# Kernel optimization log

Measured on AMD Instinct MI355X. Metric: run time of the kernel, lower is better.

Reference implementation:

```python
import jax, jax.numpy as jnp
import numpy as np

N, E = 50000, 600000
IN_DIM, HID, OUT_DIM = 128, 256, 64


def _sage_conv(x, edge_index, W_l, W_r, b):
    # PyG SAGEConv (mean aggr, root_weight=True):
    # out = mean_{j in N(i)} x_j @ W_l + x_i @ W_r + b
    src, dst = edge_index[0], edge_index[1]
    msg = x[src]  # [E, d] gather
    agg = jax.ops.segment_sum(msg, dst, num_segments=N)  # [N, d]
    cnt = jax.ops.segment_sum(jnp.ones((E,), dtype=x.dtype), dst, num_segments=N)
    agg = agg / jnp.maximum(cnt, 1.0)[:, None]
    return agg @ W_l + x @ W_r + b


def setup_inputs() -> dict:
    key = jax.random.key(0)
    ks = jax.random.split(key, 8)
    x = jax.random.normal(ks[0], (N, IN_DIM), dtype=jnp.float32)
    edge_index = jax.random.randint(ks[1], (2, E), 0, N, dtype=jnp.int64)
    s1 = 1.0 / np.sqrt(IN_DIM)
    s2 = 1.0 / np.sqrt(HID)
    W1_l = jax.random.uniform(ks[2], (IN_DIM, HID), jnp.float32, -s1, s1)
    W1_r = jax.random.uniform(ks[3], (IN_DIM, HID), jnp.float32, -s1, s1)
    b1 = jnp.zeros((HID,), jnp.float32)
    W2_l = jax.random.uniform(ks[4], (HID, OUT_DIM), jnp.float32, -s2, s2)
    W2_r = jax.random.uniform(ks[5], (HID, OUT_DIM), jnp.float32, -s2, s2)
    b2 = jnp.zeros((OUT_DIM,), jnp.float32)
    return {"x": x, "edge_index": edge_index, "W1_l": W1_l, "W1_r": W1_r,
            "b1": b1, "W2_l": W2_l, "W2_r": W2_r, "b2": b2}


def reference(x, edge_index, W1_l, W1_r, b1, W2_l, W2_r, b2):
    # SAGE.forward, eval mode (dropout = identity)
    h = jax.nn.relu(_sage_conv(x, edge_index, W1_l, W1_r, b1))
    out = _sage_conv(h, edge_index, W2_l, W2_r, b2)
    return out
```

## Files before the change

kernel.cpp:

```cpp
#include <hip/hip_runtime.h>

#define N_NODES 50000
#define N_EDGES 600000
#define N_PAD   50048
#define IN_DIM 128
#define HID 256
#define OUT_DIM 64
#define MAX_DEG 64
#define NBINS 196
#define BCAP 4096
#define NPART 256
#define ECHUNK 2344
#define EPT 10

typedef __attribute__((ext_vector_type(4))) float f32x4;
typedef __attribute__((ext_vector_type(8))) short short8;
typedef unsigned short u16;
typedef unsigned int u32;

__device__ __forceinline__ float bf2f(u32 lo16) {
  u32 u = lo16 << 16;
  return __builtin_bit_cast(float, u);
}
__device__ __forceinline__ u16 f2bf(float f) {
  u32 u = __builtin_bit_cast(u32, f);
  u = (u + 0x7FFF + ((u >> 16) & 1)) >> 16;
  return (u16)u;
}


__global__ void k_zero_gcur(int* __restrict__ gcur) {
  gcur[threadIdx.x] = 0;
}

#define SEG0 (N_PAD * 16)
#define SEG1 (SEG0 + 128 * 64)
#define SEG2 (SEG1 + 64 * 64)
#define PREP_TOT SEG2

__global__ void k_prep_part(const float* __restrict__ x,
                            const float* __restrict__ W1l, const float* __restrict__ W1r,
                            const float* __restrict__ W2l, const float* __restrict__ W2r,
                            const int* __restrict__ src, const int* __restrict__ dst,
                            u16* __restrict__ xb, u16* __restrict__ W1p,
                            u16* __restrict__ W2p, u32* __restrict__ region,
                            int* __restrict__ gcur) {
  if (blockIdx.x < NPART) {
    __shared__ int hist[256];
    __shared__ int base[256];
    const int t = threadIdx.x;
    hist[t] = 0;
    __syncthreads();
    const int e0 = blockIdx.x * ECHUNK;
    const int e1 = min(e0 + ECHUNK, N_EDGES);
    int dv[EPT], sv[EPT];
#pragma unroll
    for (int i = 0; i < EPT; ++i) {
      int e = e0 + t + i * 256;
      int ok = (e < e1);
      dv[i] = ok ? dst[e] : -1;
      sv[i] = ok ? src[e] : 0;
      if (ok) atomicAdd(&hist[dv[i] >> 8], 1);
    }
    __syncthreads();
    base[t] = (hist[t] > 0) ? atomicAdd(&gcur[t], hist[t]) : 0;
    hist[t] = 0;
    __syncthreads();
#pragma unroll
    for (int i = 0; i < EPT; ++i) {
      int d = dv[i];
      if (d >= 0) {
        int bin = d >> 8;
        int idx = base[bin] + atomicAdd(&hist[bin], 1);
        if (idx < BCAP)
          region[(size_t)bin * BCAP + idx] = (u32)(sv[i] & 0xffff) | ((u32)(d & 255) << 16);
      }
    }
    return;
  }
  int idx = (blockIdx.x - NPART) * 256 + threadIdx.x;
  if (idx < SEG0) {
    int row = idx >> 4;
    int c8 = (idx & 15) * 8;
    short8 o;
    if (row < N_NODES) {
      f32x4 a = *(const f32x4*)&x[(size_t)row * 128 + c8];
      f32x4 b = *(const f32x4*)&x[(size_t)row * 128 + c8 + 4];
      o[0] = (short)f2bf(a[0]); o[1] = (short)f2bf(a[1]);
      o[2] = (short)f2bf(a[2]); o[3] = (short)f2bf(a[3]);
      o[4] = (short)f2bf(b[0]); o[5] = (short)f2bf(b[1]);
      o[6] = (short)f2bf(b[2]); o[7] = (short)f2bf(b[3]);
    } else {
      for (int j = 0; j < 8; ++j) o[j] = 0;
    }
    *(short8*)&xb[(size_t)row * 128 + c8] = o;
  } else if (idx < SEG1) {
    int i = idx - SEG0;
    int F = i >> 6, l = i & 63;
    int wch = F >> 6, kt = (F >> 4) & 3, kk = (F >> 3) & 1, n = F & 7;
    int row = wch * 128 + n * 16 + (l & 15);
    int kb = kt * 64 + kk * 32 + (l >> 4) * 8;
    short8 o;
#pragma unroll
    for (int j = 0; j < 8; ++j) {
      int k = kb + j;
      float v = (k < 128) ? W1l[(size_t)k * HID + row] : W1r[(size_t)(k - 128) * HID + row];
      o[j] = (short)f2bf(v);
    }
    *(short8*)&W1p[(size_t)i * 8] = o;
  } else if (idx < SEG2) {
    int i = idx - SEG1;
    int G = i >> 6, l = i & 63;
    int wch = G >> 5, kk = (G >> 2) & 7, n = G & 3;
    int row = wch * 64 + n * 16 + (l & 15);
    int kb = kk * 32 + (l >> 4) * 8;
    short8 o;
#pragma unroll
    for (int j = 0; j < 8; ++j) {
      int k = kb + j;
      float v = (row < 64) ? W2l[(size_t)k * OUT_DIM + row]
                           : W2r[(size_t)k * OUT_DIM + (row - 64)];
      o[j] = (short)f2bf(v);
    }
    *(short8*)&W2p[(size_t)i * 8] = o;
  }
}


__global__ __launch_bounds__(256) void k_build(const u32* __restrict__ region,
                                               const int* __restrict__ gcur,
                                               int* __restrict__ cnt,
                                               u16* __restrict__ bucket) {
  __shared__ u16 lbkt[256 * 64];
  __shared__ int lcnt[256];
  const int t = threadIdx.x;
  const int bin = blockIdx.x;
  lcnt[t] = 0;
  __syncthreads();
  int n = gcur[bin];
  if (n > BCAP) n = BCAP;
  for (int i = t; i < n; i += 256) {
    u32 r = region[(size_t)bin * BCAP + i];
    int dl = (r >> 16) & 255;
    int pos = atomicAdd(&lcnt[dl], 1);
    if (pos < MAX_DEG) lbkt[dl * 64 + pos] = (u16)(r & 0xffff);
  }
  __syncthreads();
  int gnode = bin * 256 + t;
  if (gnode < N_NODES) cnt[gnode] = lcnt[t];
  for (int i = t; i < 2048; i += 256) {
    int nl = i >> 3, sub = i & 7;
    int gn = bin * 256 + nl;
    if (gn < N_NODES)
      *(short8*)&bucket[(size_t)gn * 64 + sub * 8] = *(const short8*)&lbkt[nl * 64 + sub * 8];
  }
}


__global__ void k_agg(const u16* __restrict__ xb, const int* __restrict__ cnt,
                      const u16* __restrict__ bucket, u16* __restrict__ agg) {
  int node = blockIdx.x * 4 + (threadIdx.x >> 6);
  if (node >= N_PAD) return;
  int lane = threadIdx.x & 63;
  int es = lane >> 4, dl = lane & 15;
  int deg = (node < N_NODES) ? cnt[node] : 0;
  int sreg = (node < N_NODES) ? (int)bucket[(size_t)node * MAX_DEG + lane] : 0;
  float acc[8] = {0.f, 0.f, 0.f, 0.f, 0.f, 0.f, 0.f, 0.f};
  short8 pend = (short8){0, 0, 0, 0, 0, 0, 0, 0};
  for (int e = 0; e < deg; e += 4) {
    int ee = e + es;
    int s = __shfl(sreg, ee & 63);
    short8 v = (short8){0, 0, 0, 0, 0, 0, 0, 0};
    if (ee < deg) v = *(const short8*)&xb[(size_t)s * 128 + dl * 8];
#pragma unroll
    for (int j = 0; j < 8; ++j) acc[j] += bf2f((u16)pend[j]);
    pend = v;
  }
#pragma unroll
  for (int j = 0; j < 8; ++j) acc[j] += bf2f((u16)pend[j]);
#pragma unroll
  for (int j = 0; j < 8; ++j) {
    acc[j] += __shfl_xor(acc[j], 16);
    acc[j] += __shfl_xor(acc[j], 32);
  }
  float inv = 1.f / fmaxf((float)deg, 1.f);
  if (es == 0) {
    short8 o;
#pragma unroll
    for (int j = 0; j < 8; ++j) o[j] = (short)f2bf(acc[j] * inv);
    *(short8*)&agg[(size_t)node * 128 + dl * 8] = o;
  }
}


__device__ __forceinline__ void gl_lds16(const void* g, void* l) {
  __builtin_amdgcn_global_load_lds((const __attribute__((address_space(1))) u32*)g,
                                   (__attribute__((address_space(3))) u32*)l, 16, 0, 0);
}

__global__ __launch_bounds__(256, 3) void k_mlp(
    const u16* __restrict__ agg, const u16* __restrict__ xb,
    const u16* __restrict__ W1p, const u16* __restrict__ W2p,
    const float* __restrict__ b1, u16* __restrict__ pb, u16* __restrict__ qb) {
  __shared__ u16 hs[64 * 256];
  __shared__ u16 As[2][64 * 64];
  const int t = threadIdx.x;
  const int wave = t >> 6;
  const int lane = t & 63;
  const int brow = blockIdx.x * 64;
  const int lr = lane & 15;
  const int kg = lane >> 4;
  const int wch = wave & 1;

  const int wr = (wave >> 1) * 32;
  const int wc = wch * 128;

  f32x4 acc[2][8];
#pragma unroll
  for (int m = 0; m < 2; ++m)
#pragma unroll
    for (int n = 0; n < 8; ++n) acc[m][n] = (f32x4){0.f, 0.f, 0.f, 0.f};

  auto stageA = [&](int buf, int kt) {
    const u16* base = (kt < 2) ? agg : xb;
    const int koff = (kt & 1) * 64;
#pragma unroll
    for (int i = 0; i < 2; ++i) {
      int chunk = wave * 2 + i;
      int f = chunk * 1024 + lane * 16;
      int row = f >> 7;
      int cbs = (f & 127) ^ ((row & 7) << 4);
      gl_lds16(&base[(size_t)(brow + row) * 128 + koff + (cbs >> 1)],
               (char*)As[buf] + chunk * 1024);
    }
  };

  stageA(0, 0);
  __syncthreads();

#pragma unroll
  for (int kt = 0; kt < 4; ++kt) {
    const int cur = kt & 1;
    if (kt < 3) stageA(cur ^ 1, kt + 1);
#pragma unroll
    for (int kk = 0; kk < 2; ++kk) {
      short8 af[2], bfr[8];
      const int cb = kk * 64 + kg * 16;
#pragma unroll
      for (int m = 0; m < 2; ++m) {
        int row = wr + m * 16 + lr;
        af[m] = *(const short8*)((const char*)As[cur] + row * 128 + (cb ^ ((row & 7) << 4)));
      }
#pragma unroll
      for (int n = 0; n < 8; ++n)
        bfr[n] = *(const short8*)&W1p[(size_t)(((wch * 4 + kt) * 2 + kk) * 8 + n) * 512 +
                                      lane * 8];
#pragma unroll
      for (int m = 0; m < 2; ++m)
#pragma unroll
        for (int n = 0; n < 8; ++n)
          acc[m][n] =
              __builtin_amdgcn_mfma_f32_16x16x32_bf16(af[m], bfr[n], acc[m][n], 0, 0, 0);
    }
    __syncthreads();
  }

#pragma unroll
  for (int n = 0; n < 8; ++n) {
    int col = wc + n * 16 + lr;
    float bv = b1[col];
#pragma unroll
    for (int m = 0; m < 2; ++m) {
#pragma unroll
      for (int j = 0; j < 4; ++j) {
        int row = wr + kg * 4 + m * 16 + j;
        float v = fmaxf(acc[m][n][j] + bv, 0.f);
        *(u16*)((char*)hs + row * 512 + ((col * 2) ^ ((row & 7) << 4))) = f2bf(v);
      }
    }
  }
  __syncthreads();

  const int wr2 = (wave >> 1) * 32;
  f32x4 acc2[2][4];
#pragma unroll
  for (int m = 0; m < 2; ++m)
#pragma unroll
    for (int n = 0; n < 4; ++n) acc2[m][n] = (f32x4){0.f, 0.f, 0.f, 0.f};

#pragma unroll
  for (int kk = 0; kk < 8; ++kk) {
    const int cb = kk * 64 + kg * 16;
    short8 af[2], bfr[4];
#pragma unroll
    for (int m = 0; m < 2; ++m) {
      int row = wr2 + m * 16 + lr;
      af[m] = *(const short8*)((const char*)hs + row * 512 + (cb ^ ((row & 7) << 4)));
    }
#pragma unroll
    for (int n = 0; n < 4; ++n)
      bfr[n] = *(const short8*)&W2p[(size_t)((wch * 8 + kk) * 4 + n) * 512 + lane * 8];
#pragma unroll
    for (int m = 0; m < 2; ++m)
#pragma unroll
      for (int n = 0; n < 4; ++n)
        acc2[m][n] =
            __builtin_amdgcn_mfma_f32_16x16x32_bf16(af[m], bfr[n], acc2[m][n], 0, 0, 0);
  }

  u16* outb = wch ? qb : pb;
#pragma unroll
  for (int n = 0; n < 4; ++n) {
    int col = n * 16 + lr;
#pragma unroll
    for (int m = 0; m < 2; ++m) {
#pragma unroll
      for (int j = 0; j < 4; ++j) {
        int row = brow + wr2 + kg * 4 + m * 16 + j;
        outb[(size_t)row * 64 + col] = f2bf(acc2[m][n][j]);
      }
    }
  }
}


__global__ void k_out(const u16* __restrict__ pb, const u16* __restrict__ qb,
                      const int* __restrict__ cnt, const u16* __restrict__ bucket,
                      const float* __restrict__ b2, float* __restrict__ out) {
  int node = blockIdx.x * 4 + (threadIdx.x >> 6);
  if (node >= N_NODES) return;
  int lane = threadIdx.x & 63;
  int es = lane >> 3, dl = lane & 7;
  int deg = cnt[node];
  int sreg = (int)bucket[(size_t)node * MAX_DEG + lane];
  float acc[8] = {0.f, 0.f, 0.f, 0.f, 0.f, 0.f, 0.f, 0.f};
  short8 pend = (short8){0, 0, 0, 0, 0, 0, 0, 0};
  for (int e = 0; e < deg; e += 8) {
    int ee = e + es;
    int s = __shfl(sreg, ee & 63);
    short8 v = (short8){0, 0, 0, 0, 0, 0, 0, 0};
    if (ee < deg) v = *(const short8*)&pb[(size_t)s * 64 + dl * 8];
#pragma unroll
    for (int j = 0; j < 8; ++j) acc[j] += bf2f((u16)pend[j]);
    pend = v;
  }
#pragma unroll
  for (int j = 0; j < 8; ++j) acc[j] += bf2f((u16)pend[j]);
#pragma unroll
  for (int j = 0; j < 8; ++j) {
    acc[j] += __shfl_xor(acc[j], 8);
    acc[j] += __shfl_xor(acc[j], 16);
    acc[j] += __shfl_xor(acc[j], 32);
  }
  float inv = 1.f / fmaxf((float)deg, 1.f);
  if (es == 0) {
    short8 q = *(const short8*)&qb[(size_t)node * 64 + dl * 8];
    f32x4 bb0 = *(const f32x4*)&b2[dl * 8];
    f32x4 bb1 = *(const f32x4*)&b2[dl * 8 + 4];
    f32x4 o0, o1;
#pragma unroll
    for (int j = 0; j < 4; ++j) {
      o0[j] = acc[j] * inv + bf2f((u16)q[j]) + bb0[j];
      o1[j] = acc[j + 4] * inv + bf2f((u16)q[j + 4]) + bb1[j];
    }
    *(f32x4*)&out[(size_t)node * 64 + dl * 8] = o0;
    *(f32x4*)&out[(size_t)node * 64 + dl * 8 + 4] = o1;
  }
}


extern "C" void kernel_launch(void* const* d_in, const int* in_sizes, int n_in,
                              void* d_out, int out_size, void* d_ws, size_t ws_size,
                              hipStream_t stream) {
  const float* x   = (const float*)d_in[0];
  const int*   ei  = (const int*)d_in[1];
  const float* W1l = (const float*)d_in[2];
  const float* W1r = (const float*)d_in[3];
  const float* b1  = (const float*)d_in[4];
  const float* W2l = (const float*)d_in[5];
  const float* W2r = (const float*)d_in[6];
  const float* b2  = (const float*)d_in[7];
  float* out = (float*)d_out;

  const int* src = ei;
  const int* dst = ei + N_EDGES;

  char* ws = (char*)d_ws;
  size_t off = 0;
  auto alloc = [&](size_t bytes) -> void* {
    void* p = ws + off;
    off = (off + bytes + 255) & ~(size_t)255;
    return p;
  };
  int* gcur   = (int*)alloc(256 * 4);
  u32* region = (u32*)alloc((size_t)NBINS * BCAP * 4);
  int* cnt    = (int*)alloc((size_t)N_NODES * 4);
  u16* bucket = (u16*)alloc((size_t)N_NODES * MAX_DEG * 2);
  u16* xb     = (u16*)alloc((size_t)N_PAD * 128 * 2);
  u16* agg    = (u16*)alloc((size_t)N_PAD * 128 * 2);
  u16* W1p    = (u16*)alloc((size_t)128 * 64 * 8 * 2);
  u16* W2p    = (u16*)alloc((size_t)64 * 64 * 8 * 2);
  u16* pb     = (u16*)alloc((size_t)N_PAD * 64 * 2);
  u16* qb     = (u16*)alloc((size_t)N_PAD * 64 * 2);

  k_zero_gcur<<<1, 256, 0, stream>>>(gcur);

  int blocks = NPART + (PREP_TOT + 255) / 256;
  k_prep_part<<<blocks, 256, 0, stream>>>(x, W1l, W1r, W2l, W2r, src, dst,
                                          xb, W1p, W2p, region, gcur);
  k_build<<<NBINS, 256, 0, stream>>>(region, gcur, cnt, bucket);
  k_agg<<<N_PAD / 4, 256, 0, stream>>>(xb, cnt, bucket, agg);
  k_mlp<<<N_PAD / 64, 256, 0, stream>>>(agg, xb, W1p, W2p, b1, pb, qb);
  k_out<<<(N_NODES + 3) / 4, 256, 0, stream>>>(pb, qb, cnt, bucket, b2, out);
}
```

Before: 98.84 us.

## Load MLP A operands directly from global and trim bucket reads/writes to degree

The first-layer GEMM in k_mlp no longer stages A tiles through double-buffered LDS with global_load_lds. Each wave now reads its A fragments straight from global memory, which removes the per-k-step barriers and frees LDS so the launch-bounds occupancy hint can rise from 3 to 5. Separately, the bucket scatter writes only the 8-wide chunks that hold valid neighbors, and the aggregation kernels read bucket entries only for lanes below the node degree, cutting memory traffic on the sparse side. The risk is that several waves now fetch the same A rows from global without LDS reuse, and that register pressure at the higher occupancy target could cause spills.

```diff
diff --git a/kernel.cpp b/kernel.cpp
--- a/kernel.cpp
+++ b/kernel.cpp
@@ -151,7 +151,7 @@
   for (int i = t; i < 2048; i += 256) {
     int nl = i >> 3, sub = i & 7;
     int gn = bin * 256 + nl;
-    if (gn < N_NODES)
+    if (gn < N_NODES && sub * 8 < lcnt[nl])
       *(short8*)&bucket[(size_t)gn * 64 + sub * 8] = *(const short8*)&lbkt[nl * 64 + sub * 8];
   }
 }
@@ -164,7 +164,7 @@
   int lane = threadIdx.x & 63;
   int es = lane >> 4, dl = lane & 15;
   int deg = (node < N_NODES) ? cnt[node] : 0;
-  int sreg = (node < N_NODES) ? (int)bucket[(size_t)node * MAX_DEG + lane] : 0;
+  int sreg = (lane < deg) ? (int)bucket[(size_t)node * MAX_DEG + lane] : 0;
   float acc[8] = {0.f, 0.f, 0.f, 0.f, 0.f, 0.f, 0.f, 0.f};
   short8 pend = (short8){0, 0, 0, 0, 0, 0, 0, 0};
   for (int e = 0; e < deg; e += 4) {
@@ -193,17 +193,11 @@
 }
 
 
-__device__ __forceinline__ void gl_lds16(const void* g, void* l) {
-  __builtin_amdgcn_global_load_lds((const __attribute__((address_space(1))) u32*)g,
-                                   (__attribute__((address_space(3))) u32*)l, 16, 0, 0);
-}
-
-__global__ __launch_bounds__(256, 3) void k_mlp(
+__global__ __launch_bounds__(256, 5) void k_mlp(
     const u16* __restrict__ agg, const u16* __restrict__ xb,
     const u16* __restrict__ W1p, const u16* __restrict__ W2p,
     const float* __restrict__ b1, u16* __restrict__ pb, u16* __restrict__ qb) {
   __shared__ u16 hs[64 * 256];
-  __shared__ u16 As[2][64 * 64];
   const int t = threadIdx.x;
   const int wave = t >> 6;
   const int lane = t & 63;
@@ -221,35 +215,17 @@
 #pragma unroll
     for (int n = 0; n < 8; ++n) acc[m][n] = (f32x4){0.f, 0.f, 0.f, 0.f};
 
-  auto stageA = [&](int buf, int kt) {
-    const u16* base = (kt < 2) ? agg : xb;
+#pragma unroll
+  for (int kt = 0; kt < 4; ++kt) {
+    const u16* Abase = (kt < 2) ? agg : xb;
     const int koff = (kt & 1) * 64;
-#pragma unroll
-    for (int i = 0; i < 2; ++i) {
-      int chunk = wave * 2 + i;
-      int f = chunk * 1024 + lane * 16;
-      int row = f >> 7;
-      int cbs = (f & 127) ^ ((row & 7) << 4);
-      gl_lds16(&base[(size_t)(brow + row) * 128 + koff + (cbs >> 1)],
-               (char*)As[buf] + chunk * 1024);
-    }
-  };
-
-  stageA(0, 0);
-  __syncthreads();
-
-#pragma unroll
-  for (int kt = 0; kt < 4; ++kt) {
-    const int cur = kt & 1;
-    if (kt < 3) stageA(cur ^ 1, kt + 1);
 #pragma unroll
     for (int kk = 0; kk < 2; ++kk) {
       short8 af[2], bfr[8];
-      const int cb = kk * 64 + kg * 16;
 #pragma unroll
       for (int m = 0; m < 2; ++m) {
-        int row = wr + m * 16 + lr;
-        af[m] = *(const short8*)((const char*)As[cur] + row * 128 + (cb ^ ((row & 7) << 4)));
+        int row = brow + wr + m * 16 + lr;
+        af[m] = *(const short8*)&Abase[(size_t)row * 128 + koff + kk * 32 + kg * 8];
       }
 #pragma unroll
       for (int n = 0; n < 8; ++n)
@@ -262,7 +238,6 @@
           acc[m][n] =
               __builtin_amdgcn_mfma_f32_16x16x32_bf16(af[m], bfr[n], acc[m][n], 0, 0, 0);
     }
-    __syncthreads();
   }
 
 #pragma unroll
@@ -332,7 +307,7 @@
   int lane = threadIdx.x & 63;
   int es = lane >> 3, dl = lane & 7;
   int deg = cnt[node];
-  int sreg = (int)bucket[(size_t)node * MAX_DEG + lane];
+  int sreg = (lane < deg) ? (int)bucket[(size_t)node * MAX_DEG + lane] : 0;
   float acc[8] = {0.f, 0.f, 0.f, 0.f, 0.f, 0.f, 0.f, 0.f};
   short8 pend = (short8){0, 0, 0, 0, 0, 0, 0, 0};
   for (int e = 0; e < deg; e += 8) {
```

New measurement: 139.2 us. 1.41x slower.
